# Optimization experiments

Measured on AMD Instinct MI355X. Metric: run time of the kernel, lower is better.

## Reference

```python
import jax, jax.numpy as jnp
import numpy as np


def _pairwise_dist(pred, gt):
    # pred: [B, N, 3], gt: [B, M, 3] -> Euclidean distances [B, N, M]
    p2 = jnp.sum(pred * pred, axis=-1)  # [B, N]
    g2 = jnp.sum(gt * gt, axis=-1)      # [B, M]
    cross = jnp.einsum('bnd,bmd->bnm', pred, gt)  # [B, N, M]
    d2 = p2[:, :, None] + g2[:, None, :] - 2.0 * cross
    return jnp.sqrt(jnp.maximum(d2, 1e-12))


def setup_inputs() -> dict:
    key = jax.random.key(0)
    k1, k2 = jax.random.split(key)
    pred = jax.random.normal(k1, (32, 4096, 3), dtype=jnp.float32)
    gt = jax.random.normal(k2, (32, 4096, 3), dtype=jnp.float32)
    return {"pred": pred, "gt": gt}


def reference(pred, gt):
    dist = _pairwise_dist(pred, gt)              # [B, N, M]
    chamfer1 = jnp.mean(jnp.min(dist, axis=1))   # min over pred points (dim=1)
    chamfer2 = jnp.mean(jnp.min(dist, axis=2))   # min over gt points (dim=2)
    return chamfer1 + chamfer2
```

## Files before the change

### kernel.cpp

```cpp
#include <hip/hip_runtime.h>
#include <math.h>


typedef short short8 __attribute__((ext_vector_type(8)));
typedef float f32x16 __attribute__((ext_vector_type(16)));
typedef unsigned int uint;

#define NPTS  4096
#define TPBM  512
#define TPBP  256
#define NPANEL 16
#define GRID_MAIN (32 * NPANEL)
#define NBT   128
#define CHT   16
#define NCH   4
#define ONEB ((short)0x3F80)

__device__ __forceinline__ unsigned short bf16h(float f) {
    uint u = __float_as_uint(f);
    uint r = u + 0x7FFFu + ((u >> 16) & 1u);
    return (unsigned short)(r >> 16);
}
__device__ __forceinline__ float bf16f(unsigned short h) {
    return __uint_as_float(((uint)h) << 16);
}
struct Split2 { unsigned short h, m; };
__device__ __forceinline__ Split2 split2(float x) {
    Split2 s;
    s.h = bf16h(x);
    s.m = bf16h(x - bf16f(s.h));
    return s;
}

__global__ __launch_bounds__(TPBP) void chamfer_prep(
    const float* __restrict__ pred, short8* __restrict__ Bfrag,
    uint* __restrict__ wspred)
{
    const int gid = blockIdx.x * TPBP + threadIdx.x;
    if (gid < 32 * NPTS) wspred[gid] = 0xFFFFFFFFu;

    const int lane = gid & 63;
    const int ent  = gid >> 6;
    const int b    = ent >> 7;
    const int tile = ent & 127;
    const int c31  = lane & 31, half = lane >> 5;

    const float* p = pred + ((size_t)(b * NPTS + tile * 32 + c31)) * 3;
    float x = p[0], y = p[1], z = p[2];
    Split2 X = split2(x), Y = split2(y), Z = split2(z);
    Split2 P2 = split2(fmaf(x, x, fmaf(y, y, z * z)));

    short8 f;
    if (half == 0) {
        f[0]=(short)X.h; f[1]=(short)Y.h; f[2]=(short)Z.h;
        f[3]=(short)X.m; f[4]=(short)Y.m; f[5]=(short)Z.m;
        f[6]=(short)X.h; f[7]=(short)Y.h;
    } else {
        f[0]=(short)Z.h; f[1]=(short)X.m; f[2]=(short)Y.m; f[3]=(short)Z.m;
        f[4]=ONEB;       f[5]=ONEB;       f[6]=(short)P2.h; f[7]=(short)P2.m;
    }
    Bfrag[gid] = f;
}

__global__ __launch_bounds__(TPBM, 4) void chamfer_mfma(
    const float* __restrict__ gt,
    uint* __restrict__ wspred,
    float* __restrict__ wsgt,
    const short8* __restrict__ Bfrag)
{
    const int bx    = blockIdx.x;
    const int b     = bx >> 4;
    const int panel = bx & 15;
    const int tid   = threadIdx.x;
    const int lane  = tid & 63, wid = tid >> 6;
    const int rw    = wid >> 1;
    const int cq    = wid & 1;
    const int c31   = lane & 31, half = lane >> 5;

    __shared__ short8 sB[2 * CHT * 64];
    __shared__ uint   sPmin[NPTS];
    __shared__ float  sred[256 * 2];
    __shared__ float  sw[8];

    for (int c = tid; c < NPTS; c += TPBM) sPmin[c] = 0x7F7FFFFFu;

    const float* gtb = gt + (size_t)b * NPTS * 3;
    short8 afr[2];
    float gm[2][16];
#pragma unroll
    for (int fr = 0; fr < 2; ++fr) {
        const int row = panel * 256 + rw * 64 + fr * 32 + c31;
        const float* ap = gtb + (size_t)row * 3;
        float x = ap[0], y = ap[1], z = ap[2];
        Split2 X = split2(-2.0f*x), Y = split2(-2.0f*y), Z = split2(-2.0f*z);
        Split2 G2 = split2(fmaf(x, x, fmaf(y, y, z * z)));
        short8 a;
        if (half == 0) {
            a[0]=(short)X.h; a[1]=(short)Y.h; a[2]=(short)Z.h;
            a[3]=(short)X.h; a[4]=(short)Y.h; a[5]=(short)Z.h;
            a[6]=(short)X.m; a[7]=(short)Y.m;
        } else {
            a[0]=(short)Z.m; a[1]=(short)X.m; a[2]=(short)Y.m; a[3]=(short)Z.m;
            a[4]=(short)G2.h; a[5]=(short)G2.m; a[6]=ONEB; a[7]=ONEB;
        }
        afr[fr] = a;
#pragma unroll
        for (int r = 0; r < 16; ++r) gm[fr][r] = 1e30f;
    }

    const size_t bfb = (size_t)b * (NBT * 64);
    const f32x16 zero = {0.f,0.f,0.f,0.f,0.f,0.f,0.f,0.f,
                         0.f,0.f,0.f,0.f,0.f,0.f,0.f,0.f};

    short8 pf[4];
#pragma unroll
    for (int ps = 0; ps < 4; ++ps) {
        const int u = ps * TPBM + tid;
        const int ucq = u >> 10, ut = (u >> 6) & 15, ul = u & 63;
        pf[ps] = Bfrag[bfb + (size_t)((ucq * 64 + ut) * 64 + ul)];
    }

    for (int ch = 0; ch < NCH; ++ch) {
        __syncthreads();
#pragma unroll
        for (int ps = 0; ps < 4; ++ps) sB[ps * TPBM + tid] = pf[ps];
        __syncthreads();

        const int chn = (ch + 1 < NCH) ? ch + 1 : ch;
#pragma unroll
        for (int ps = 0; ps < 4; ++ps) {
            const int u = ps * TPBM + tid;
            const int ucq = u >> 10, ut = (u >> 6) & 15, ul = u & 63;
            pf[ps] = Bfrag[bfb + (size_t)((ucq * 64 + chn * CHT + ut) * 64 + ul)];
        }

#pragma unroll 2
        for (int t = 0; t < CHT; ++t) {
            short8 bfr = sB[(cq * CHT + t) * 64 + lane];
            f32x16 a0 = __builtin_amdgcn_mfma_f32_32x32x16_bf16(
                afr[0], bfr, zero, 0, 0, 0);
            f32x16 a1 = __builtin_amdgcn_mfma_f32_32x32x16_bf16(
                afr[1], bfr, zero, 0, 0, 0);

            float pmin = 1e30f;
#pragma unroll
            for (int r = 0; r < 16; ++r) {
                gm[0][r] = fminf(gm[0][r], a0[r]);
                gm[1][r] = fminf(gm[1][r], a1[r]);
                pmin = fminf(fminf(a0[r], a1[r]), pmin);
            }
            atomicMin(&sPmin[cq * 2048 + (ch * CHT + t) * 32 + c31],
                      __float_as_uint(fmaxf(pmin, 1e-12f)));
        }
    }
    __syncthreads();

    uint* wsb = wspred + (size_t)b * NPTS;
    for (int c = tid; c < NPTS; c += TPBM) {
        const uint mine = sPmin[c];
        if (mine < wsb[c]) atomicMin(&wsb[c], mine);
    }

#pragma unroll
    for (int off = 1; off < 32; off <<= 1)
#pragma unroll
        for (int fr = 0; fr < 2; ++fr)
#pragma unroll
            for (int r = 0; r < 16; ++r)
                gm[fr][r] = fminf(gm[fr][r], __shfl_xor(gm[fr][r], off, 64));
    if (c31 == 0) {
#pragma unroll
        for (int fr = 0; fr < 2; ++fr)
#pragma unroll
            for (int r = 0; r < 16; ++r)
                sred[(rw*64 + fr*32 + (r&3) + 8*(r>>2) + 4*half) * 2 + cq]
                    = gm[fr][r];
    }
    __syncthreads();

    float ssum = 0.0f;
    if (tid < 256) {
        float v = fminf(sred[tid * 2], sred[tid * 2 + 1]);
        ssum = sqrtf(fmaxf(v, 1e-12f));
    }
#pragma unroll
    for (int off = 32; off > 0; off >>= 1) ssum += __shfl_down(ssum, off, 64);
    if (lane == 0) sw[wid] = ssum;
    __syncthreads();
    if (tid == 0)
        wsgt[bx] = sw[0]+sw[1]+sw[2]+sw[3]+sw[4]+sw[5]+sw[6]+sw[7];
}

__global__ __launch_bounds__(TPBP) void chamfer_finish(
    const uint* __restrict__ wspred, const float* __restrict__ wsgt,
    float* __restrict__ out)
{
    __shared__ float swv[TPBP / 64];
    const int tid  = threadIdx.x;
    const int base = blockIdx.x * (TPBP * 4) + tid;

    float s = 0.0f;
#pragma unroll
    for (int r = 0; r < 4; ++r)
        s += sqrtf(__uint_as_float(wspred[base + r * TPBP]));
    if (blockIdx.x == 0) {
#pragma unroll
        for (int r = 0; r < 2; ++r)
            s += wsgt[tid + r * TPBP];
    }

#pragma unroll
    for (int off = 32; off > 0; off >>= 1) s += __shfl_down(s, off, 64);
    const int wid = tid >> 6, lane = tid & 63;
    if (lane == 0) swv[wid] = s;
    __syncthreads();
    if (tid == 0) {
        float tot = swv[0] + swv[1] + swv[2] + swv[3];
        atomicAdd(out, tot * (1.0f / 131072.0f));
    }
}

extern "C" void kernel_launch(void* const* d_in, const int* in_sizes, int n_in,
                              void* d_out, int out_size, void* d_ws, size_t ws_size,
                              hipStream_t stream)
{
    const float* pred = (const float*)d_in[0];
    const float* gt   = (const float*)d_in[1];
    float* out        = (float*)d_out;

    uint*   wspred = (uint*)d_ws;
    float*  wsgt   = (float*)((char*)d_ws + (512 << 10));
    short8* Bfrag  = (short8*)((char*)d_ws + (1 << 20));

    hipMemsetAsync(d_out, 0, sizeof(float), stream);

    chamfer_prep<<<dim3((32 * NBT * 64) / TPBP), dim3(TPBP), 0, stream>>>(
        pred, Bfrag, wspred);
    chamfer_mfma<<<dim3(GRID_MAIN), dim3(TPBM), 0, stream>>>(
        gt, wspred, wsgt, Bfrag);
    chamfer_finish<<<dim3(128), dim3(TPBP), 0, stream>>>(wspred, wsgt, out);
}
```

Measured before the change: 101.8 us.

## Compute both Chamfer directions as separate row-min passes, dropping column-min atomics

Instead of deriving the per-pred minimum from column reductions with shared and global atomicMin, the main kernel now runs two independent directions (gt-as-query and pred-as-query), each doing only row-wise minima in registers. The prep kernel builds B fragments for both point sets, and the finish kernel becomes a single block that writes the result directly, with no memset or atomics. This removes per-tile cross-lane pmin reductions, shared atomics, the 16KB sPmin buffer and the global atomic merge. In exchange it doubles the MFMA work.

```diff
diff --git a/kernel.cpp b/kernel.cpp
--- a/kernel.cpp
+++ b/kernel.cpp
@@ -9,10 +9,10 @@
 #define NPTS  4096
 #define TPBM  512
 #define TPBP  256
-#define NPANEL 16
-#define GRID_MAIN (32 * NPANEL)
+#define NPANEL 8
+#define GRID_MAIN (2 * 32 * NPANEL)
 #define NBT   128
-#define CHT   16
+#define CHT   32
 #define NCH   4
 #define ONEB ((short)0x3F80)
 
@@ -33,22 +33,22 @@
 }
 
 __global__ __launch_bounds__(TPBP) void chamfer_prep(
-    const float* __restrict__ pred, short8* __restrict__ Bfrag,
-    uint* __restrict__ wspred)
-{
-    const int gid = blockIdx.x * TPBP + threadIdx.x;
-    if (gid < 32 * NPTS) wspred[gid] = 0xFFFFFFFFu;
-
+    const float* __restrict__ pred, const float* __restrict__ gt,
+    short8* __restrict__ Bfrag)
+{
+    const int gid  = blockIdx.x * TPBP + threadIdx.x;
     const int lane = gid & 63;
     const int ent  = gid >> 6;
-    const int b    = ent >> 7;
+    const int side = ent >> 12;
+    const int b    = (ent >> 7) & 31;
     const int tile = ent & 127;
     const int c31  = lane & 31, half = lane >> 5;
 
-    const float* p = pred + ((size_t)(b * NPTS + tile * 32 + c31)) * 3;
+    const float* src = side ? gt : pred;
+    const float* p = src + ((size_t)(b * NPTS + tile * 32 + c31)) * 3;
     float x = p[0], y = p[1], z = p[2];
     Split2 X = split2(x), Y = split2(y), Z = split2(z);
-    Split2 P2 = split2(fmaf(x, x, fmaf(y, y, z * z)));
+    Split2 T2 = split2(fmaf(x, x, fmaf(y, y, z * z)));
 
     short8 f;
     if (half == 0) {
@@ -57,43 +57,41 @@
         f[6]=(short)X.h; f[7]=(short)Y.h;
     } else {
         f[0]=(short)Z.h; f[1]=(short)X.m; f[2]=(short)Y.m; f[3]=(short)Z.m;
-        f[4]=ONEB;       f[5]=ONEB;       f[6]=(short)P2.h; f[7]=(short)P2.m;
+        f[4]=ONEB;       f[5]=ONEB;       f[6]=(short)T2.h; f[7]=(short)T2.m;
     }
     Bfrag[gid] = f;
 }
 
 __global__ __launch_bounds__(TPBM, 4) void chamfer_mfma(
+    const float* __restrict__ pred,
     const float* __restrict__ gt,
-    uint* __restrict__ wspred,
     float* __restrict__ wsgt,
     const short8* __restrict__ Bfrag)
 {
     const int bx    = blockIdx.x;
-    const int b     = bx >> 4;
-    const int panel = bx & 15;
+    const int dir   = bx >> 8;
+    const int rem   = bx & 255;
+    const int b     = rem >> 3;
+    const int panel = rem & 7;
     const int tid   = threadIdx.x;
     const int lane  = tid & 63, wid = tid >> 6;
-    const int rw    = wid >> 1;
-    const int cq    = wid & 1;
     const int c31   = lane & 31, half = lane >> 5;
 
-    __shared__ short8 sB[2 * CHT * 64];
-    __shared__ uint   sPmin[NPTS];
-    __shared__ float  sred[256 * 2];
+    __shared__ short8 sB[CHT * 64];
     __shared__ float  sw[8];
 
-    for (int c = tid; c < NPTS; c += TPBM) sPmin[c] = 0x7F7FFFFFu;
-
-    const float* gtb = gt + (size_t)b * NPTS * 3;
+    const float* qsrc = (dir ? pred : gt) + (size_t)b * NPTS * 3;
+    const size_t bfb  = ((size_t)dir * 32 + b) * (NBT * 64);
+
     short8 afr[2];
     float gm[2][16];
 #pragma unroll
     for (int fr = 0; fr < 2; ++fr) {
-        const int row = panel * 256 + rw * 64 + fr * 32 + c31;
-        const float* ap = gtb + (size_t)row * 3;
+        const int row = panel * 512 + wid * 64 + fr * 32 + c31;
+        const float* ap = qsrc + (size_t)row * 3;
         float x = ap[0], y = ap[1], z = ap[2];
         Split2 X = split2(-2.0f*x), Y = split2(-2.0f*y), Z = split2(-2.0f*z);
-        Split2 G2 = split2(fmaf(x, x, fmaf(y, y, z * z)));
+        Split2 Q2 = split2(fmaf(x, x, fmaf(y, y, z * z)));
         short8 a;
         if (half == 0) {
             a[0]=(short)X.h; a[1]=(short)Y.h; a[2]=(short)Z.h;
@@ -101,14 +99,13 @@
             a[6]=(short)X.m; a[7]=(short)Y.m;
         } else {
             a[0]=(short)Z.m; a[1]=(short)X.m; a[2]=(short)Y.m; a[3]=(short)Z.m;
-            a[4]=(short)G2.h; a[5]=(short)G2.m; a[6]=ONEB; a[7]=ONEB;
+            a[4]=(short)Q2.h; a[5]=(short)Q2.m; a[6]=ONEB; a[7]=ONEB;
         }
         afr[fr] = a;
 #pragma unroll
         for (int r = 0; r < 16; ++r) gm[fr][r] = 1e30f;
     }
 
-    const size_t bfb = (size_t)b * (NBT * 64);
     const f32x16 zero = {0.f,0.f,0.f,0.f,0.f,0.f,0.f,0.f,
                          0.f,0.f,0.f,0.f,0.f,0.f,0.f,0.f};
 
@@ -116,8 +113,7 @@
 #pragma unroll
     for (int ps = 0; ps < 4; ++ps) {
         const int u = ps * TPBM + tid;
-        const int ucq = u >> 10, ut = (u >> 6) & 15, ul = u & 63;
-        pf[ps] = Bfrag[bfb + (size_t)((ucq * 64 + ut) * 64 + ul)];
+        pf[ps] = Bfrag[bfb + (size_t)u];
     }
 
     for (int ch = 0; ch < NCH; ++ch) {
@@ -130,35 +126,22 @@
 #pragma unroll
         for (int ps = 0; ps < 4; ++ps) {
             const int u = ps * TPBM + tid;
-            const int ucq = u >> 10, ut = (u >> 6) & 15, ul = u & 63;
-            pf[ps] = Bfrag[bfb + (size_t)((ucq * 64 + chn * CHT + ut) * 64 + ul)];
+            pf[ps] = Bfrag[bfb + (size_t)(chn * (CHT * 64) + u)];
         }
 
-#pragma unroll 2
+#pragma unroll 4
         for (int t = 0; t < CHT; ++t) {
-            short8 bfr = sB[(cq * CHT + t) * 64 + lane];
+            short8 bfr = sB[t * 64 + lane];
             f32x16 a0 = __builtin_amdgcn_mfma_f32_32x32x16_bf16(
                 afr[0], bfr, zero, 0, 0, 0);
             f32x16 a1 = __builtin_amdgcn_mfma_f32_32x32x16_bf16(
                 afr[1], bfr, zero, 0, 0, 0);
-
-            float pmin = 1e30f;
 #pragma unroll
             for (int r = 0; r < 16; ++r) {
                 gm[0][r] = fminf(gm[0][r], a0[r]);
                 gm[1][r] = fminf(gm[1][r], a1[r]);
-                pmin = fminf(fminf(a0[r], a1[r]), pmin);
             }
-            atomicMin(&sPmin[cq * 2048 + (ch * CHT + t) * 32 + c31],
-                      __float_as_uint(fmaxf(pmin, 1e-12f)));
         }
-    }
-    __syncthreads();
-
-    uint* wsb = wspred + (size_t)b * NPTS;
-    for (int c = tid; c < NPTS; c += TPBM) {
-        const uint mine = sPmin[c];
-        if (mine < wsb[c]) atomicMin(&wsb[c], mine);
     }
 
 #pragma unroll
@@ -168,56 +151,40 @@
 #pragma unroll
             for (int r = 0; r < 16; ++r)
                 gm[fr][r] = fminf(gm[fr][r], __shfl_xor(gm[fr][r], off, 64));
+
+    float s = 0.0f;
     if (c31 == 0) {
 #pragma unroll
         for (int fr = 0; fr < 2; ++fr)
 #pragma unroll
             for (int r = 0; r < 16; ++r)
-                sred[(rw*64 + fr*32 + (r&3) + 8*(r>>2) + 4*half) * 2 + cq]
-                    = gm[fr][r];
-    }
-    __syncthreads();
-
-    float ssum = 0.0f;
-    if (tid < 256) {
-        float v = fminf(sred[tid * 2], sred[tid * 2 + 1]);
-        ssum = sqrtf(fmaxf(v, 1e-12f));
-    }
-#pragma unroll
-    for (int off = 32; off > 0; off >>= 1) ssum += __shfl_down(ssum, off, 64);
-    if (lane == 0) sw[wid] = ssum;
+                s += sqrtf(fmaxf(gm[fr][r], 1e-12f));
+    }
+    s += __shfl_xor(s, 32, 64);
+    if (lane == 0) sw[wid] = s;
     __syncthreads();
     if (tid == 0)
         wsgt[bx] = sw[0]+sw[1]+sw[2]+sw[3]+sw[4]+sw[5]+sw[6]+sw[7];
 }
 
 __global__ __launch_bounds__(TPBP) void chamfer_finish(
-    const uint* __restrict__ wspred, const float* __restrict__ wsgt,
-    float* __restrict__ out)
+    const float* __restrict__ wsgt, float* __restrict__ out)
 {
     __shared__ float swv[TPBP / 64];
-    const int tid  = threadIdx.x;
-    const int base = blockIdx.x * (TPBP * 4) + tid;
+    const int tid = threadIdx.x;
 
     float s = 0.0f;
 #pragma unroll
-    for (int r = 0; r < 4; ++r)
-        s += sqrtf(__uint_as_float(wspred[base + r * TPBP]));
-    if (blockIdx.x == 0) {
-#pragma unroll
-        for (int r = 0; r < 2; ++r)
-            s += wsgt[tid + r * TPBP];
-    }
+    for (int r = 0; r < GRID_MAIN / TPBP; ++r)
+        s += wsgt[tid + r * TPBP];
 
 #pragma unroll
     for (int off = 32; off > 0; off >>= 1) s += __shfl_down(s, off, 64);
     const int wid = tid >> 6, lane = tid & 63;
     if (lane == 0) swv[wid] = s;
     __syncthreads();
-    if (tid == 0) {
-        float tot = swv[0] + swv[1] + swv[2] + swv[3];
-        atomicAdd(out, tot * (1.0f / 131072.0f));
-    }
+    if (tid == 0)
+        out[0] = (swv[0] + swv[1] + swv[2] + swv[3]) * (1.0f / 131072.0f);
 }
 
 extern "C" void kernel_launch(void* const* d_in, const int* in_sizes, int n_in,
@@ -228,15 +195,12 @@
     const float* gt   = (const float*)d_in[1];
     float* out        = (float*)d_out;
 
-    uint*   wspred = (uint*)d_ws;
-    float*  wsgt   = (float*)((char*)d_ws + (512 << 10));
-    short8* Bfrag  = (short8*)((char*)d_ws + (1 << 20));
-
-    hipMemsetAsync(d_out, 0, sizeof(float), stream);
-
-    chamfer_prep<<<dim3((32 * NBT * 64) / TPBP), dim3(TPBP), 0, stream>>>(
-        pred, Bfrag, wspred);
+    float*  wsgt  = (float*)d_ws;
+    short8* Bfrag = (short8*)((char*)d_ws + (1 << 20));
+
+    chamfer_prep<<<dim3((2 * 32 * NBT * 64) / TPBP), dim3(TPBP), 0, stream>>>(
+        pred, gt, Bfrag);
     chamfer_mfma<<<dim3(GRID_MAIN), dim3(TPBM), 0, stream>>>(
-        gt, wspred, wsgt, Bfrag);
-    chamfer_finish<<<dim3(128), dim3(TPBP), 0, stream>>>(wspred, wsgt, out);
-}
+        pred, gt, wsgt, Bfrag);
+    chamfer_finish<<<dim3(1), dim3(TPBP), 0, stream>>>(wsgt, out);
+}
```

New measurement: 105.8 us. 4.0% more time.
